# Kernel optimization log

Hardware: AMD Instinct MI355X
Metric: run time of the kernel (lower is better)

## Reference

```python
import jax, jax.numpy as jnp
import numpy as np

B, N = 8, 48
NEMBED, EMBED_DIM, HID_DIM = 1000, 32, 32
IN_DIM = EMBED_DIM + 1  # feature dim after concatenating xfeat
N_OPS = 8  # exchangeable 3-tensor basis: identity + means over each nonempty axis subset


def setup_inputs() -> dict:
    key = jax.random.key(0)
    k1, k2, k3, k4, k5 = jax.random.split(key, 5)
    xcat = jax.random.randint(k1, (B, N), 0, NEMBED)
    xfeat = jax.random.normal(k2, (B, N), dtype=jnp.float32)
    embed_table = jax.random.normal(k3, (NEMBED, EMBED_DIM), dtype=jnp.float32)
    # SetEq3to3 coefficients: (in_dim, n_basis_ops, out_dim), Glorot-ish scale
    coefs = jax.random.normal(k4, (IN_DIM, N_OPS, HID_DIM), dtype=jnp.float32) * np.sqrt(2.0 / (IN_DIM + HID_DIM))
    eq_bias = jnp.zeros((HID_DIM,), dtype=jnp.float32)
    out_w = jax.random.normal(k5, (HID_DIM, 1), dtype=jnp.float32) * np.sqrt(1.0 / HID_DIM)
    out_b = jnp.zeros((1,), dtype=jnp.float32)
    return {"xcat": xcat, "xfeat": xfeat, "embed_table": embed_table,
            "coefs": coefs, "eq_bias": eq_bias, "out_w": out_w, "out_b": out_b}


def _set_eq3to3(t, coefs, eq_bias):
    # t: (B, d, n, n, n); coefs: (d, 8, h). Each basis op is a mean over a
    # subset of the three set axes (kept as size-1 dims so broadcasting restores shape).
    def mix(op, s):
        return jnp.einsum('bd...,dh->bh...', op, coefs[:, s, :])
    m_i = t.mean(axis=2, keepdims=True)
    m_j = t.mean(axis=3, keepdims=True)
    m_k = t.mean(axis=4, keepdims=True)
    m_ij = m_i.mean(axis=3, keepdims=True)
    m_ik = m_i.mean(axis=4, keepdims=True)
    m_jk = m_j.mean(axis=4, keepdims=True)
    m_ijk = m_ij.mean(axis=4, keepdims=True)
    out = (mix(t, 0) + mix(m_i, 1) + mix(m_j, 2) + mix(m_k, 3)
           + mix(m_ij, 4) + mix(m_ik, 5) + mix(m_jk, 6) + mix(m_ijk, 7))
    return out + eq_bias.reshape(1, -1, 1, 1, 1)  # (B, h, n, n, n)


def reference(xcat, xfeat, embed_table, coefs, eq_bias, out_w, out_b):
    e = embed_table[xcat]                                   # (B, n, d_e)
    x = jnp.concatenate([e, xfeat[..., None]], axis=-1)      # (B, n, d) with d = d_e + 1
    t = jnp.einsum('bid,bjd,bkd->bdijk', x, x, x)            # (B, d, n, n, n)
    y = _set_eq3to3(t, coefs, eq_bias)                       # (B, h, n, n, n)
    y = jnp.transpose(y, (0, 2, 3, 4, 1))                    # (B, n, n, n, h)
    y = jax.nn.relu(y)
    y = y.mean(axis=(1, 2, 3))                               # (B, h) mean pool
    y = jax.nn.relu(y)
    # dropout is inactive in eval mode (training=False)
    return y @ out_w + out_b                                 # (B, 1)
```

## Files before the change

### kernel.cpp

```cpp
#include <hip/hip_runtime.h>
#include <cstdint>
#include <cstddef>

#define BB 8
#define NN 48
#define DD 33
#define KP 128
#define HH 32
#define MM (NN*NN)
#define NC (NN*HH)
#define TILE 96
#define TM (MM/TILE)
#define TN (NC/TILE)
#define LDK 136

typedef __attribute__((ext_vector_type(8))) _Float16 f16x8;
typedef __attribute__((ext_vector_type(4))) float f32x4;

__global__ void k_setup(const int* __restrict__ xcat, const float* __restrict__ xfeat,
                        const float* __restrict__ embed, float* __restrict__ xw,
                        float* __restrict__ sw, float* __restrict__ hsum) {
    int b = blockIdx.x, t = threadIdx.x;
    for (int idx = t; idx < NN * DD; idx += 256) {
        int i = idx / DD, d = idx - i * DD;
        float v = (d < 32) ? embed[xcat[b * NN + i] * 32 + d] : xfeat[b * NN + i];
        xw[b * NN * DD + idx] = v;
    }
    if (t < HH) hsum[b * HH + t] = 0.f;
    __syncthreads();
    if (t < DD) {
        float a = 0.f;
        for (int i = 0; i < NN; ++i) a += xw[b * NN * DD + i * DD + t];
        sw[b * DD + t] = a * (1.0f / 48.0f);
    }
}

__global__ void k_build(const float* __restrict__ xw, const float* __restrict__ sw,
                        const float* __restrict__ coefs, const float* __restrict__ eq_bias,
                        _Float16* __restrict__ Pw, _Float16* __restrict__ Dw) {
    int idx = blockIdx.x * 256 + threadIdx.x;
    int rb = idx >> 4, chunk = idx & 15, d0 = chunk * 8;
    if (rb < BB * MM) {
        int b = rb / MM, row = rb % MM;
        int i = row / NN, j = row - i * NN;
        const float* xi = xw + (b * NN + i) * DD;
        const float* xj = xw + (b * NN + j) * DD;
        const float* sb = sw + b * DD;
        f16x8 v;
        for (int e = 0; e < 8; ++e) {
            int dp = d0 + e; float r = 0.f;
            if (dp < 33)                    r = xi[dp] * xj[dp];
            else if (dp >= 40 && dp < 73)   r = xi[dp - 40] * sb[dp - 40];
            else if (dp >= 80 && dp < 113)  r = xj[dp - 80] * sb[dp - 80];
            else if (dp == 120)             r = 1.f;
            v[e] = (_Float16)r;
        }
        *(f16x8*)&Pw[(size_t)rb * KP + d0] = v;
    } else {
        int rb2 = rb - BB * MM;
        int b = rb2 / NC, n = rb2 % NC;
        int k = n >> 5, h = n & 31;
        const float* xk = xw + (b * NN + k) * DD;
        const float* sb = sw + b * DD;
        f16x8 v;
        for (int e = 0; e < 8; ++e) {
            int dp = d0 + e; float r = 0.f;
            if (dp < 33) {
                int d = dp;
                r = coefs[(d * 8 + 0) * HH + h] * xk[d] + coefs[(d * 8 + 3) * HH + h] * sb[d];
            } else if (dp >= 40 && dp < 73) {
                int d = dp - 40;
                r = coefs[(d * 8 + 2) * HH + h] * xk[d] + coefs[(d * 8 + 6) * HH + h] * sb[d];
            } else if (dp >= 80 && dp < 113) {
                int d = dp - 80;
                r = coefs[(d * 8 + 1) * HH + h] * xk[d] + coefs[(d * 8 + 5) * HH + h] * sb[d];
            } else if (dp == 120) {
                float g = 0.f;
                for (int d = 0; d < DD; ++d) {
                    float sd = sb[d];
                    g += sd * sd * (coefs[(d * 8 + 4) * HH + h] * xk[d]
                                  + coefs[(d * 8 + 7) * HH + h] * sd);
                }
                r = g + eq_bias[h];
            }
            v[e] = (_Float16)r;
        }
        *(f16x8*)&Dw[(size_t)rb2 * KP + d0] = v;
    }
}

__global__ __launch_bounds__(256) void k_gemm(const _Float16* __restrict__ Pw,
                                              const _Float16* __restrict__ Dw,
                                              float* __restrict__ hsum) {
    __shared__ __align__(16) _Float16 As[TILE][LDK];
    __shared__ __align__(16) _Float16 Bs[TILE][LDK];
    __shared__ float hacc[HH];
    int t = threadIdx.x;
    int bx = blockIdx.x, by = blockIdx.y, b = blockIdx.z;
    int M0 = by * TILE, N0 = bx * TILE;
    if (t < HH) hacc[t] = 0.f;

    const _Float16* Pg = Pw + ((size_t)b * MM + M0) * KP;
    const _Float16* Dg = Dw + ((size_t)b * NC + N0) * KP;
    for (int c = 0; c < 6; ++c) {
        int ch = c * 256 + t;
        int row = ch >> 4, col = (ch & 15) * 8;
        *(f16x8*)&As[row][col] = *(const f16x8*)(Pg + row * KP + col);
        *(f16x8*)&Bs[row][col] = *(const f16x8*)(Dg + row * KP + col);
    }
    __syncthreads();

    int lane = t & 63, wave = t >> 6;
    int wm = (wave >> 1) * 48, wn = (wave & 1) * 48;
    int lrow = lane & 15, quad = lane >> 4;

    f32x4 acc[3][3];
    for (int mt = 0; mt < 3; ++mt)
        for (int nt = 0; nt < 3; ++nt)
            acc[mt][nt] = (f32x4){0.f, 0.f, 0.f, 0.f};

    for (int ks = 0; ks < 4; ++ks) {
        f16x8 af[3], bf[3];
        for (int mt = 0; mt < 3; ++mt)
            af[mt] = *(const f16x8*)&As[wm + mt * 16 + lrow][ks * 32 + quad * 8];
        for (int nt = 0; nt < 3; ++nt)
            bf[nt] = *(const f16x8*)&Bs[wn + nt * 16 + lrow][ks * 32 + quad * 8];
        for (int mt = 0; mt < 3; ++mt)
            for (int nt = 0; nt < 3; ++nt)
                acc[mt][nt] = __builtin_amdgcn_mfma_f32_16x16x32_f16(af[mt], bf[nt], acc[mt][nt], 0, 0, 0);
    }

    float fs[3] = {0.f, 0.f, 0.f};
    for (int mt = 0; mt < 3; ++mt)
        for (int nt = 0; nt < 3; ++nt)
            for (int r = 0; r < 4; ++r)
                fs[nt] += fmaxf(acc[mt][nt][r], 0.f);
    for (int nt = 0; nt < 3; ++nt) {
        int h = (N0 + wn + nt * 16 + lrow) & 31;
        atomicAdd(&hacc[h], fs[nt]);
    }
    __syncthreads();
    if (t < HH) atomicAdd(&hsum[b * HH + t], hacc[t]);
}

__global__ void k_final(const float* __restrict__ hsum, const float* __restrict__ out_w,
                        const float* __restrict__ out_b, float* __restrict__ out) {
    __shared__ float red[BB * HH];
    int t = threadIdx.x;
    int h = t & 31;
    red[t] = fmaxf(hsum[t] * (1.0f / 110592.0f), 0.f) * out_w[h];
    __syncthreads();
    if (t < BB) {
        float a = 0.f;
        for (int x = 0; x < HH; ++x) a += red[t * HH + x];
        out[t] = a + out_b[0];
    }
}

extern "C" void kernel_launch(void* const* d_in, const int* in_sizes, int n_in,
                              void* d_out, int out_size, void* d_ws, size_t ws_size,
                              hipStream_t stream) {
    (void)in_sizes; (void)n_in; (void)out_size; (void)ws_size;
    const int*   xcat    = (const int*)d_in[0];
    const float* xfeat   = (const float*)d_in[1];
    const float* embed   = (const float*)d_in[2];
    const float* coefs   = (const float*)d_in[3];
    const float* eq_bias = (const float*)d_in[4];
    const float* out_w   = (const float*)d_in[5];
    const float* out_b   = (const float*)d_in[6];
    float* out = (float*)d_out;

    char* w = (char*)d_ws;
    float*    xw   = (float*)(w + 0);
    float*    sw   = (float*)(w + 51200);
    float*    hsum = (float*)(w + 52480);
    _Float16* Pw   = (_Float16*)(w + 53760);
    _Float16* Dw   = (_Float16*)(w + 4772352);

    k_setup<<<dim3(BB), dim3(256), 0, stream>>>(xcat, xfeat, embed, xw, sw, hsum);
    k_build<<<dim3(1920), dim3(256), 0, stream>>>(xw, sw, coefs, eq_bias, Pw, Dw);
    k_gemm<<<dim3(TN, TM, BB), dim3(256), 0, stream>>>(Pw, Dw, hsum);
    k_final<<<dim3(1), dim3(256), 0, stream>>>(hsum, out_w, out_b, out);
}
```

Measured before the change: 125.8 us.

## Build pairwise P operand on the fly inside GEMM instead of materializing it

The pairwise-product A operand is no longer written to global memory by a separate build kernel. The GEMM now computes each tile directly from padded x and mean vectors while loading shared memory. The coefficient tensor is transposed once into a padded, vectorizable layout so the D-operand build can use vector loads. This removes a large global write and read-back of the P matrix, at the cost of recomputing P tiles in each GEMM block that shares an M range.

Result: no change. 125.9 us (+0.1%).

```diff
diff --git a/kernel.cpp b/kernel.cpp
--- a/kernel.cpp
+++ b/kernel.cpp
@@ -5,6 +5,7 @@
 #define BB 8
 #define NN 48
 #define DD 33
+#define XS 40
 #define KP 128
 #define HH 32
 #define MM (NN*NN)
@@ -18,78 +19,73 @@
 typedef __attribute__((ext_vector_type(4))) float f32x4;
 
 __global__ void k_setup(const int* __restrict__ xcat, const float* __restrict__ xfeat,
-                        const float* __restrict__ embed, float* __restrict__ xw,
-                        float* __restrict__ sw, float* __restrict__ hsum) {
+                        const float* __restrict__ embed, const float* __restrict__ coefs,
+                        float* __restrict__ xw, float* __restrict__ sw,
+                        float* __restrict__ ct, float* __restrict__ hsum) {
     int b = blockIdx.x, t = threadIdx.x;
-    for (int idx = t; idx < NN * DD; idx += 256) {
-        int i = idx / DD, d = idx - i * DD;
-        float v = (d < 32) ? embed[xcat[b * NN + i] * 32 + d] : xfeat[b * NN + i];
-        xw[b * NN * DD + idx] = v;
-    }
-    if (t < HH) hsum[b * HH + t] = 0.f;
-    __syncthreads();
-    if (t < DD) {
-        float a = 0.f;
-        for (int i = 0; i < NN; ++i) a += xw[b * NN * DD + i * DD + t];
-        sw[b * DD + t] = a * (1.0f / 48.0f);
+    if (b < BB) {
+        for (int idx = t; idx < NN * XS; idx += 256) {
+            int i = idx / XS, d = idx - i * XS;
+            float v = 0.f;
+            if (d < 32)       v = embed[xcat[b * NN + i] * 32 + d];
+            else if (d == 32) v = xfeat[b * NN + i];
+            xw[b * NN * XS + idx] = v;
+        }
+        if (t < HH) hsum[b * HH + t] = 0.f;
+        __syncthreads();
+        if (t < XS) {
+            float a = 0.f;
+            for (int i = 0; i < NN; ++i) a += xw[b * NN * XS + i * XS + t];
+            sw[b * XS + t] = a * (1.0f / 48.0f);
+        }
+    } else {
+        for (int idx = t; idx < 8 * HH * XS; idx += 256) {
+            int qh = idx / XS, d = idx - qh * XS;
+            int q = qh >> 5, h = qh & 31;
+            ct[idx] = (d < DD) ? coefs[(d * 8 + q) * HH + h] : 0.f;
+        }
     }
 }
 
-__global__ void k_build(const float* __restrict__ xw, const float* __restrict__ sw,
-                        const float* __restrict__ coefs, const float* __restrict__ eq_bias,
-                        _Float16* __restrict__ Pw, _Float16* __restrict__ Dw) {
+__global__ void k_buildD(const float* __restrict__ xw, const float* __restrict__ sw,
+                         const float* __restrict__ ct, const float* __restrict__ eq_bias,
+                         _Float16* __restrict__ Dw) {
     int idx = blockIdx.x * 256 + threadIdx.x;
-    int rb = idx >> 4, chunk = idx & 15, d0 = chunk * 8;
-    if (rb < BB * MM) {
-        int b = rb / MM, row = rb % MM;
-        int i = row / NN, j = row - i * NN;
-        const float* xi = xw + (b * NN + i) * DD;
-        const float* xj = xw + (b * NN + j) * DD;
-        const float* sb = sw + b * DD;
-        f16x8 v;
-        for (int e = 0; e < 8; ++e) {
-            int dp = d0 + e; float r = 0.f;
-            if (dp < 33)                    r = xi[dp] * xj[dp];
-            else if (dp >= 40 && dp < 73)   r = xi[dp - 40] * sb[dp - 40];
-            else if (dp >= 80 && dp < 113)  r = xj[dp - 80] * sb[dp - 80];
-            else if (dp == 120)             r = 1.f;
-            v[e] = (_Float16)r;
+    int rowid = idx >> 4, d0 = (idx & 15) * 8;
+    int b = rowid / NC, n = rowid - b * NC;
+    int k = n >> 5, h = n & 31;
+    const float* xk = xw + (b * NN + k) * XS;
+    const float* sb = sw + b * XS;
+    f16x8 v;
+    if (d0 < 120) {
+        int seg = (d0 >= 80) ? 2 : (d0 >= 40) ? 1 : 0;
+        int d = d0 - seg * 40;
+        const int QA[3] = {0, 2, 1}, QB[3] = {3, 6, 5};
+        const float* ca = ct + (QA[seg] * HH + h) * XS + d;
+        const float* cb = ct + (QB[seg] * HH + h) * XS + d;
+        f32x4 ca0 = *(const f32x4*)(ca),     ca1 = *(const f32x4*)(ca + 4);
+        f32x4 cb0 = *(const f32x4*)(cb),     cb1 = *(const f32x4*)(cb + 4);
+        f32x4 xk0 = *(const f32x4*)(xk + d), xk1 = *(const f32x4*)(xk + d + 4);
+        f32x4 sb0 = *(const f32x4*)(sb + d), sb1 = *(const f32x4*)(sb + d + 4);
+        f32x4 r0 = ca0 * xk0 + cb0 * sb0;
+        f32x4 r1 = ca1 * xk1 + cb1 * sb1;
+        for (int e = 0; e < 4; ++e) { v[e] = (_Float16)r0[e]; v[4 + e] = (_Float16)r1[e]; }
+    } else {
+        const float* c4 = ct + (4 * HH + h) * XS;
+        const float* c7 = ct + (7 * HH + h) * XS;
+        float g = 0.f;
+        for (int d = 0; d < DD; ++d) {
+            float sd = sb[d];
+            g += sd * sd * (c4[d] * xk[d] + c7[d] * sd);
         }
-        *(f16x8*)&Pw[(size_t)rb * KP + d0] = v;
-    } else {
-        int rb2 = rb - BB * MM;
-        int b = rb2 / NC, n = rb2 % NC;
-        int k = n >> 5, h = n & 31;
-        const float* xk = xw + (b * NN + k) * DD;
-        const float* sb = sw + b * DD;
-        f16x8 v;
-        for (int e = 0; e < 8; ++e) {
-            int dp = d0 + e; float r = 0.f;
-            if (dp < 33) {
-                int d = dp;
-                r = coefs[(d * 8 + 0) * HH + h] * xk[d] + coefs[(d * 8 + 3) * HH + h] * sb[d];
-            } else if (dp >= 40 && dp < 73) {
-                int d = dp - 40;
-                r = coefs[(d * 8 + 2) * HH + h] * xk[d] + coefs[(d * 8 + 6) * HH + h] * sb[d];
-            } else if (dp >= 80 && dp < 113) {
-                int d = dp - 80;
-                r = coefs[(d * 8 + 1) * HH + h] * xk[d] + coefs[(d * 8 + 5) * HH + h] * sb[d];
-            } else if (dp == 120) {
-                float g = 0.f;
-                for (int d = 0; d < DD; ++d) {
-                    float sd = sb[d];
-                    g += sd * sd * (coefs[(d * 8 + 4) * HH + h] * xk[d]
-                                  + coefs[(d * 8 + 7) * HH + h] * sd);
-                }
-                r = g + eq_bias[h];
-            }
-            v[e] = (_Float16)r;
-        }
-        *(f16x8*)&Dw[(size_t)rb2 * KP + d0] = v;
+        v = (f16x8){0, 0, 0, 0, 0, 0, 0, 0};
+        v[0] = (_Float16)(g + eq_bias[h]);
     }
+    *(f16x8*)&Dw[(size_t)rowid * KP + d0] = v;
 }
 
-__global__ __launch_bounds__(256) void k_gemm(const _Float16* __restrict__ Pw,
+__global__ __launch_bounds__(256) void k_gemm(const float* __restrict__ xw,
+                                              const float* __restrict__ sw,
                                               const _Float16* __restrict__ Dw,
                                               float* __restrict__ hsum) {
     __shared__ __align__(16) _Float16 As[TILE][LDK];
@@ -100,13 +96,31 @@
     int M0 = by * TILE, N0 = bx * TILE;
     if (t < HH) hacc[t] = 0.f;
 
-    const _Float16* Pg = Pw + ((size_t)b * MM + M0) * KP;
-    const _Float16* Dg = Dw + ((size_t)b * NC + N0) * KP;
+    const _Float16* Dg = Dw + ((size_t)(b * NC + N0)) * KP;
+    const float* xb = xw + b * NN * XS;
+    const float* sb = sw + b * XS;
+
     for (int c = 0; c < 6; ++c) {
         int ch = c * 256 + t;
-        int row = ch >> 4, col = (ch & 15) * 8;
-        *(f16x8*)&As[row][col] = *(const f16x8*)(Pg + row * KP + col);
-        *(f16x8*)&Bs[row][col] = *(const f16x8*)(Dg + row * KP + col);
+        int row = ch >> 4, d0 = (ch & 15) * 8;
+        *(f16x8*)&Bs[row][d0] = *(const f16x8*)(Dg + row * KP + d0);
+        int grow = M0 + row;
+        int i = grow / NN, j = grow - i * NN;
+        f16x8 v;
+        if (d0 < 120) {
+            int seg = (d0 >= 80) ? 2 : (d0 >= 40) ? 1 : 0;
+            int d = d0 - seg * 40;
+            const float* p1 = (seg == 2) ? (xb + j * XS) : (xb + i * XS);
+            const float* p2 = (seg == 0) ? (xb + j * XS) : sb;
+            f32x4 a0 = *(const f32x4*)(p1 + d), a1 = *(const f32x4*)(p1 + d + 4);
+            f32x4 b0 = *(const f32x4*)(p2 + d), b1 = *(const f32x4*)(p2 + d + 4);
+            f32x4 r0 = a0 * b0, r1 = a1 * b1;
+            for (int e = 0; e < 4; ++e) { v[e] = (_Float16)r0[e]; v[4 + e] = (_Float16)r1[e]; }
+        } else {
+            v = (f16x8){0, 0, 0, 0, 0, 0, 0, 0};
+            v[0] = (_Float16)1.f;
+        }
+        *(f16x8*)&As[row][d0] = v;
     }
     __syncthreads();
 
@@ -172,13 +186,13 @@
 
     char* w = (char*)d_ws;
     float*    xw   = (float*)(w + 0);
-    float*    sw   = (float*)(w + 51200);
-    float*    hsum = (float*)(w + 52480);
-    _Float16* Pw   = (_Float16*)(w + 53760);
-    _Float16* Dw   = (_Float16*)(w + 4772352);
+    float*    sw   = (float*)(w + 61440);
+    float*    ct   = (float*)(w + 62720);
+    float*    hsum = (float*)(w + 103680);
+    _Float16* Dw   = (_Float16*)(w + 104704);
 
-    k_setup<<<dim3(BB), dim3(256), 0, stream>>>(xcat, xfeat, embed, xw, sw, hsum);
-    k_build<<<dim3(1920), dim3(256), 0, stream>>>(xw, sw, coefs, eq_bias, Pw, Dw);
-    k_gemm<<<dim3(TN, TM, BB), dim3(256), 0, stream>>>(Pw, Dw, hsum);
+    k_setup<<<dim3(BB + 1), dim3(256), 0, stream>>>(xcat, xfeat, embed, coefs, xw, sw, ct, hsum);
+    k_buildD<<<dim3(768), dim3(256), 0, stream>>>(xw, sw, ct, eq_bias, Dw);
+    k_gemm<<<dim3(TN, TM, BB), dim3(256), 0, stream>>>(xw, sw, Dw, hsum);
     k_final<<<dim3(1), dim3(256), 0, stream>>>(hsum, out_w, out_b, out);
 }
```
